# Kernel tuning notes

Hardware: AMD Instinct MI355X
Metric: run time of the kernel (lower is better)

The kernel has to match this reference:

```python
import jax, jax.numpy as jnp
import numpy as np

B, N, K = 8192, 2048, 4  # batch, nodes, neighbors (original: 45, 168, 4)


def _collect_and_transfer(x, adj):
    # x: (B, N), adj: (N, K) int indices of neighbors.
    # Original builds, per node i, a (B, K) block of gathered neighbor values,
    # stacks to (N, B, K), then raw-reshapes (view) to (B, 1, K, N).
    g = jnp.transpose(x[:, adj], (1, 0, 2))   # (N, B, K)
    return g.reshape(x.shape[0], 1, K, adj.shape[0])  # memory reinterpretation, as in .view


def reference(x, label, adj, conv_w, conv_b, lin_w, lin_b):
    a = jnp.concatenate([_collect_and_transfer(x, adj),
                         _collect_and_transfer(label, adj)], axis=1)  # (B, 2, K, N)
    # Conv2d(2 -> 1, kernel=(1,4), stride=(1,4)): (B, 1, K, N//4)
    y = jax.lax.conv_general_dilated(
        a, conv_w, window_strides=(1, 4), padding='VALID',
        dimension_numbers=('NCHW', 'OIHW', 'NCHW'))
    y = jax.nn.relu(y + conv_b[None, :, None, None])
    y = y.reshape(B, N)              # K * (N//4) == N
    return y @ lin_w.T + lin_b       # Linear(N, N)


def setup_inputs() -> dict:
    key = jax.random.key(0)
    k1, k2, k3, k4, k5 = jax.random.split(key, 5)
    return {
        'x': jax.random.normal(k1, (B, N), dtype=jnp.float32),
        'label': jax.random.normal(k2, (B, N), dtype=jnp.float32),
        'adj': jax.random.randint(k3, (N, K), 0, N, dtype=jnp.int32),
        'conv_w': jax.random.normal(k4, (1, 2, 1, 4), dtype=jnp.float32) * 0.1,
        'conv_b': jnp.zeros((1,), dtype=jnp.float32),
        'lin_w': jax.random.normal(k5, (N, N), dtype=jnp.float32) * 0.02,
        'lin_b': jnp.zeros((N,), dtype=jnp.float32),
    }
```

## Files before the change

### kernel.cpp

```cpp
#include <hip/hip_runtime.h>

typedef __bf16 bf16;
typedef bf16 bf16x8 __attribute__((ext_vector_type(8)));
typedef float f32x4 __attribute__((ext_vector_type(4)));
typedef unsigned short ushort;
typedef ushort ushort4v __attribute__((ext_vector_type(4)));

#define BB 8192
#define NN 2048

__device__ __forceinline__ void async16(const void* g, void* l) {
    __builtin_amdgcn_global_load_lds(
        (__attribute__((address_space(1))) void*)(void*)g,
        (__attribute__((address_space(3))) void*)l,
        16, 0, 0);
}

__global__ __launch_bounds__(256) void conv_gather(
    const float* __restrict__ x, const float* __restrict__ label,
    const int* __restrict__ adj, const float* __restrict__ cw,
    const float* __restrict__ cb, bf16* __restrict__ V) {
    __shared__ float4 sxl[NN];
    const int bb0 = blockIdx.x * 2;
    const int t   = threadIdx.x;

    const float4* x0 = (const float4*)(x     + (size_t)bb0 * NN);
    const float4* x1 = (const float4*)(x     + (size_t)(bb0 + 1) * NN);
    const float4* l0 = (const float4*)(label + (size_t)bb0 * NN);
    const float4* l1 = (const float4*)(label + (size_t)(bb0 + 1) * NN);
#pragma unroll
    for (int q = 0; q < 2; ++q) {
        int i = q * 256 + t;
        float4 a = x0[i], b = l0[i], c = x1[i], d = l1[i];
        sxl[i*4+0] = make_float4(a.x, b.x, c.x, d.x);
        sxl[i*4+1] = make_float4(a.y, b.y, c.y, d.y);
        sxl[i*4+2] = make_float4(a.z, b.z, c.z, d.z);
        sxl[i*4+3] = make_float4(a.w, b.w, c.w, d.w);
    }
    const float w0 = cw[0], w1 = cw[1], w2 = cw[2], w3 = cw[3];
    const float w4 = cw[4], w5 = cw[5], w6 = cw[6], w7 = cw[7];
    const float bias = cb[0];

    const int4* adj4 = (const int4*)adj;
    int4 a[8];
#pragma unroll
    for (int j = 0; j < 8; ++j) a[j] = adj4[t * 8 + j];

    __syncthreads();

    bf16 o0[8], o1[8];
#pragma unroll
    for (int j = 0; j < 8; ++j) {
        int4 aa = a[j];
        float4 p0 = sxl[aa.x];
        float4 p1 = sxl[aa.y];
        float4 p2 = sxl[aa.z];
        float4 p3 = sxl[aa.w];
        float v0 = bias
                 + w0 * p0.x + w1 * p1.x + w2 * p2.x + w3 * p3.x
                 + w4 * p0.y + w5 * p1.y + w6 * p2.y + w7 * p3.y;
        float v1 = bias
                 + w0 * p0.z + w1 * p1.z + w2 * p2.z + w3 * p3.z
                 + w4 * p0.w + w5 * p1.w + w6 * p2.w + w7 * p3.w;
        o0[j] = (bf16)fmaxf(v0, 0.0f);
        o1[j] = (bf16)fmaxf(v1, 0.0f);
    }
    *(bf16x8*)(V + (size_t)bb0 * NN + t * 8)       = *(const bf16x8*)o0;
    *(bf16x8*)(V + (size_t)(bb0 + 1) * NN + t * 8) = *(const bf16x8*)o1;
}

__global__ __launch_bounds__(256) void transp_cvtw(
    const ushort* __restrict__ V, ushort* __restrict__ Y,
    const float* __restrict__ W, bf16* __restrict__ Wb) {
    const int b = blockIdx.x;
    if (b >= 4096) {
        size_t i = (size_t)(b - 4096) * 256 + threadIdx.x;
        float4 v0 = ((const float4*)W)[i * 2 + 0];
        float4 v1 = ((const float4*)W)[i * 2 + 1];
        bf16x8 o;
        o[0] = (bf16)v0.x; o[1] = (bf16)v0.y; o[2] = (bf16)v0.z; o[3] = (bf16)v0.w;
        o[4] = (bf16)v1.x; o[5] = (bf16)v1.y; o[6] = (bf16)v1.z; o[7] = (bf16)v1.w;
        ((bf16x8*)Wb)[i] = o;
        return;
    }
    __shared__ ushort tile[64][68];
    const int g0 = (b & 31) * 64;
    const int p0 = (b >> 5) * 64;
    const int c  = threadIdx.x & 15;
    const int r4 = threadIdx.x >> 4;

#pragma unroll
    for (int pass = 0; pass < 4; ++pass) {
        int r = pass * 16 + r4;
        ushort4v v = *(const ushort4v*)(V + (size_t)(p0 + r) * NN + g0 + c * 4);
        *(ushort4v*)&tile[r][c * 4] = v;
    }
    __syncthreads();
#pragma unroll
    for (int pass = 0; pass < 4; ++pass) {
        int r = pass * 16 + r4;
        ushort4v o;
        o.x = tile[c * 4 + 0][r];
        o.y = tile[c * 4 + 1][r];
        o.z = tile[c * 4 + 2][r];
        o.w = tile[c * 4 + 3][r];
        *(ushort4v*)(Y + (size_t)(g0 + r) * BB + p0 + c * 4) = o;
    }
}

__global__ __launch_bounds__(256) void gemm_bt(
    const bf16* __restrict__ A, const bf16* __restrict__ W,
    const float* __restrict__ bias, float* __restrict__ out) {
    __shared__ __attribute__((aligned(16))) bf16 sA[2][128 * 32];
    __shared__ __attribute__((aligned(16))) bf16 sB[2][128 * 32];

    const int t    = threadIdx.x;
    const int lane = t & 63;
    const int wv   = t >> 6;
    const int wm   = wv & 1;
    const int wn   = wv >> 1;
    const int m0   = blockIdx.x * 128;
    const int n0   = blockIdx.y * 128;

    f32x4 acc[4][4] = {};

    const int r  = t >> 2;
    const int c8 = (t & 3) * 8;
    const bf16* gA0 = A + (size_t)(m0 + r)      * 2048 + c8;
    const bf16* gA1 = A + (size_t)(m0 + r + 64) * 2048 + c8;
    const bf16* gB0 = W + (size_t)(n0 + r)      * 2048 + c8;
    const bf16* gB1 = W + (size_t)(n0 + r + 64) * 2048 + c8;
    bf16* lA0[2], *lA1[2], *lB0[2], *lB1[2];
#pragma unroll
    for (int s = 0; s < 2; ++s) {
        lA0[s] = sA[s] + (wv * 16)      * 32;
        lA1[s] = sA[s] + (64 + wv * 16) * 32;
        lB0[s] = sB[s] + (wv * 16)      * 32;
        lB1[s] = sB[s] + (64 + wv * 16) * 32;
    }

    const int quad = lane >> 4;
    const int l16  = lane & 15;
    const int foff = (wm * 64 + l16) * 32 + quad * 8;
    const int goff = (wn * 64 + l16) * 32 + quad * 8;

    for (int k0 = 0; k0 < 2048; k0 += 64) {
#pragma unroll
        for (int s = 0; s < 2; ++s) {
            async16(gA0 + k0 + s * 32, lA0[s]);
            async16(gA1 + k0 + s * 32, lA1[s]);
            async16(gB0 + k0 + s * 32, lB0[s]);
            async16(gB1 + k0 + s * 32, lB1[s]);
        }
        __syncthreads();

#pragma unroll
        for (int s = 0; s < 2; ++s) {
            const bf16* fA = sA[s] + foff;
            const bf16* fB = sB[s] + goff;
            bf16x8 af[4], bfr[4];
#pragma unroll
            for (int i = 0; i < 4; ++i) af[i]  = *(const bf16x8*)(fA + i * 16 * 32);
#pragma unroll
            for (int j = 0; j < 4; ++j) bfr[j] = *(const bf16x8*)(fB + j * 16 * 32);
#pragma unroll
            for (int i = 0; i < 4; ++i)
#pragma unroll
                for (int j = 0; j < 4; ++j)
                    acc[i][j] = __builtin_amdgcn_mfma_f32_16x16x32_bf16(
                        af[i], bfr[j], acc[i][j], 0, 0, 0);
        }
        __syncthreads();
    }

#pragma unroll
    for (int j = 0; j < 4; ++j) {
        int col = n0 + wn * 64 + j * 16 + l16;
        float bcol = bias[col];
#pragma unroll
        for (int i = 0; i < 4; ++i) {
            int rowb = m0 + wm * 64 + i * 16 + quad * 4;
#pragma unroll
            for (int rr = 0; rr < 4; ++rr) {
                out[(size_t)(rowb + rr) * 2048 + col] = acc[i][j][rr] + bcol;
            }
        }
    }
}

extern "C" void kernel_launch(void* const* d_in, const int* in_sizes, int n_in,
                              void* d_out, int out_size, void* d_ws, size_t ws_size,
                              hipStream_t stream) {
    (void)in_sizes; (void)n_in; (void)out_size; (void)ws_size;
    const float* x     = (const float*)d_in[0];
    const float* label = (const float*)d_in[1];
    const int*   adj   = (const int*)d_in[2];
    const float* cw    = (const float*)d_in[3];
    const float* cb    = (const float*)d_in[4];
    const float* lw    = (const float*)d_in[5];
    const float* lb    = (const float*)d_in[6];
    float* out = (float*)d_out;

    bf16* V  = (bf16*)d_out;
    bf16* Y2 = (bf16*)d_ws;
    bf16* Wb = (bf16*)((char*)d_ws + (size_t)2048 * 8192 * 2);

    conv_gather<<<BB / 2, 256, 0, stream>>>(x, label, adj, cw, cb, V);
    transp_cvtw<<<6144, 256, 0, stream>>>((const ushort*)V, (ushort*)Y2,
                                          lw, Wb);
    gemm_bt<<<dim3(64, 16), 256, 0, stream>>>(Y2, Wb, lb, out);
}
```

Baseline: 281.7 us.

## Rewrite GEMM with 256x256 tiles, 8 waves, swizzled LDS and interleaved prefetch

The GEMM moves from 128x128 tiles with 4 waves to 256x256 tiles with 8 waves and K-steps of 64. It uses XOR-swizzled LDS layouts and a hand-scheduled double buffer that interleaves async global-to-LDS loads with MFMA phases, using explicit barriers, waitcnts and setprio. The gather kernel also XOR-swizzles its shared-memory table to reduce bank conflicts on random neighbour reads. The larger tile raises arithmetic intensity, but the grid shrinks to 256 blocks and register pressure rises, which may leave CUs underused.

```diff
diff --git a/kernel.cpp b/kernel.cpp
--- a/kernel.cpp
+++ b/kernel.cpp
@@ -32,10 +32,12 @@
     for (int q = 0; q < 2; ++q) {
         int i = q * 256 + t;
         float4 a = x0[i], b = l0[i], c = x1[i], d = l1[i];
-        sxl[i*4+0] = make_float4(a.x, b.x, c.x, d.x);
-        sxl[i*4+1] = make_float4(a.y, b.y, c.y, d.y);
-        sxl[i*4+2] = make_float4(a.z, b.z, c.z, d.z);
-        sxl[i*4+3] = make_float4(a.w, b.w, c.w, d.w);
+        int n0i = i * 4;
+        int sx  = (i >> 1) & 7;
+        sxl[(n0i + 0) ^ sx] = make_float4(a.x, b.x, c.x, d.x);
+        sxl[(n0i + 1) ^ sx] = make_float4(a.y, b.y, c.y, d.y);
+        sxl[(n0i + 2) ^ sx] = make_float4(a.z, b.z, c.z, d.z);
+        sxl[(n0i + 3) ^ sx] = make_float4(a.w, b.w, c.w, d.w);
     }
     const float w0 = cw[0], w1 = cw[1], w2 = cw[2], w3 = cw[3];
     const float w4 = cw[4], w5 = cw[5], w6 = cw[6], w7 = cw[7];
@@ -52,10 +54,10 @@
 #pragma unroll
     for (int j = 0; j < 8; ++j) {
         int4 aa = a[j];
-        float4 p0 = sxl[aa.x];
-        float4 p1 = sxl[aa.y];
-        float4 p2 = sxl[aa.z];
-        float4 p3 = sxl[aa.w];
+        float4 p0 = sxl[aa.x ^ ((aa.x >> 3) & 7)];
+        float4 p1 = sxl[aa.y ^ ((aa.y >> 3) & 7)];
+        float4 p2 = sxl[aa.z ^ ((aa.z >> 3) & 7)];
+        float4 p3 = sxl[aa.w ^ ((aa.w >> 3) & 7)];
         float v0 = bias
                  + w0 * p0.x + w1 * p1.x + w2 * p2.x + w3 * p3.x
                  + w4 * p0.y + w5 * p1.y + w6 * p2.y + w7 * p3.y;
@@ -108,84 +110,182 @@
     }
 }
 
-__global__ __launch_bounds__(256) void gemm_bt(
+__global__ __launch_bounds__(512, 2) void gemm_bt(
     const bf16* __restrict__ A, const bf16* __restrict__ W,
     const float* __restrict__ bias, float* __restrict__ out) {
-    __shared__ __attribute__((aligned(16))) bf16 sA[2][128 * 32];
-    __shared__ __attribute__((aligned(16))) bf16 sB[2][128 * 32];
+    __shared__ __attribute__((aligned(16))) bf16 sA[2][16384];
+    __shared__ __attribute__((aligned(16))) bf16 sB[2][16384];
 
     const int t    = threadIdx.x;
     const int lane = t & 63;
     const int wv   = t >> 6;
     const int wm   = wv & 1;
     const int wn   = wv >> 1;
-    const int m0   = blockIdx.x * 128;
-    const int n0   = blockIdx.y * 128;
-
-    f32x4 acc[4][4] = {};
-
-    const int r  = t >> 2;
-    const int c8 = (t & 3) * 8;
-    const bf16* gA0 = A + (size_t)(m0 + r)      * 2048 + c8;
-    const bf16* gA1 = A + (size_t)(m0 + r + 64) * 2048 + c8;
-    const bf16* gB0 = W + (size_t)(n0 + r)      * 2048 + c8;
-    const bf16* gB1 = W + (size_t)(n0 + r + 64) * 2048 + c8;
-    bf16* lA0[2], *lA1[2], *lB0[2], *lB1[2];
-#pragma unroll
-    for (int s = 0; s < 2; ++s) {
-        lA0[s] = sA[s] + (wv * 16)      * 32;
-        lA1[s] = sA[s] + (64 + wv * 16) * 32;
-        lB0[s] = sB[s] + (wv * 16)      * 32;
-        lB1[s] = sB[s] + (64 + wv * 16) * 32;
-    }
-
-    const int quad = lane >> 4;
     const int l16  = lane & 15;
-    const int foff = (wm * 64 + l16) * 32 + quad * 8;
-    const int goff = (wn * 64 + l16) * 32 + quad * 8;
-
-    for (int k0 = 0; k0 < 2048; k0 += 64) {
-#pragma unroll
-        for (int s = 0; s < 2; ++s) {
-            async16(gA0 + k0 + s * 32, lA0[s]);
-            async16(gA1 + k0 + s * 32, lA1[s]);
-            async16(gB0 + k0 + s * 32, lB0[s]);
-            async16(gB1 + k0 + s * 32, lB1[s]);
+    const int l4   = lane >> 4;
+
+    const int bx = blockIdx.x >> 3;
+    const int by = blockIdx.x & 7;
+    const int m0 = bx * 256;
+    const int n0 = by * 256;
+
+    const int r8  = t >> 3;
+    const int c8  = ((t & 7) ^ (r8 & 7)) * 8;
+    const int dst = t * 8;
+
+    const int sw    = l16 & 7;
+    const int aOff0 = (wm * 128 + l16) * 64 + ((l4    ) ^ sw) * 8;
+    const int aOff1 = (wm * 128 + l16) * 64 + ((l4 + 4) ^ sw) * 8;
+    const int bOff0 = (wn * 64  + l16) * 64 + ((l4    ) ^ sw) * 8;
+    const int bOff1 = (wn * 64  + l16) * 64 + ((l4 + 4) ^ sw) * 8;
+
+    f32x4  acc[8][4] = {};
+    bf16x8 aR[4][2], bR[4][2];
+
+#define GBAR()  asm volatile("s_barrier" ::: "memory")
+#define LGKM0() asm volatile("s_waitcnt lgkmcnt(0)" ::: "memory")
+#define VMW4()  asm volatile("s_waitcnt vmcnt(4)" ::: "memory")
+#define VMW0()  asm volatile("s_waitcnt vmcnt(0)" ::: "memory")
+
+#define STG(G, rb, kt, lp) do {                                           \
+        const bf16* _s = (G) + (size_t)((rb) + r8) * 2048 + (kt) + c8;    \
+        async16(_s, (lp) + dst);                                          \
+        async16(_s + (size_t)64 * 2048, (lp) + 4096 + dst);               \
+    } while (0)
+
+#define LDA(sp, mh) do {                                                  \
+        const bf16* _p = (sp) + (mh) * 4096;                              \
+        aR[0][0] = *(const bf16x8*)(_p + aOff0);                          \
+        aR[0][1] = *(const bf16x8*)(_p + aOff1);                          \
+        aR[1][0] = *(const bf16x8*)(_p + 1024 + aOff0);                   \
+        aR[1][1] = *(const bf16x8*)(_p + 1024 + aOff1);                   \
+        aR[2][0] = *(const bf16x8*)(_p + 2048 + aOff0);                   \
+        aR[2][1] = *(const bf16x8*)(_p + 2048 + aOff1);                   \
+        aR[3][0] = *(const bf16x8*)(_p + 3072 + aOff0);                   \
+        aR[3][1] = *(const bf16x8*)(_p + 3072 + aOff1);                   \
+    } while (0)
+
+#define LDB(sp, nh) do {                                                  \
+        const bf16* _p = (sp) + (nh) * 2048;                              \
+        bR[(nh)*2+0][0] = *(const bf16x8*)(_p + bOff0);                   \
+        bR[(nh)*2+0][1] = *(const bf16x8*)(_p + bOff1);                   \
+        bR[(nh)*2+1][0] = *(const bf16x8*)(_p + 1024 + bOff0);            \
+        bR[(nh)*2+1][1] = *(const bf16x8*)(_p + 1024 + bOff1);            \
+    } while (0)
+
+#define MM(mh, nh) do {                                                   \
+        __builtin_amdgcn_s_setprio(1);                                    \
+        _Pragma("unroll")                                                 \
+        for (int _mf = 0; _mf < 4; ++_mf)                                 \
+            _Pragma("unroll")                                             \
+            for (int _nf = 0; _nf < 2; ++_nf) {                           \
+                acc[(mh)*4+_mf][(nh)*2+_nf] =                             \
+                    __builtin_amdgcn_mfma_f32_16x16x32_bf16(              \
+                        aR[_mf][0], bR[(nh)*2+_nf][0],                    \
+                        acc[(mh)*4+_mf][(nh)*2+_nf], 0, 0, 0);            \
+                acc[(mh)*4+_mf][(nh)*2+_nf] =                             \
+                    __builtin_amdgcn_mfma_f32_16x16x32_bf16(              \
+                        aR[_mf][1], bR[(nh)*2+_nf][1],                    \
+                        acc[(mh)*4+_mf][(nh)*2+_nf], 0, 0, 0);            \
+            }                                                             \
+        __builtin_amdgcn_s_setprio(0);                                    \
+    } while (0)
+
+    bf16* const sA0 = &sA[0][0]; bf16* const sA1 = &sA[1][0];
+    bf16* const sB0 = &sB[0][0]; bf16* const sB1 = &sB[1][0];
+
+    STG(A, m0,       0,  sA0);
+    STG(A, m0 + 128, 0,  sA0 + 8192);
+    STG(W, n0,       0,  sB0);
+    STG(W, n0 + 128, 0,  sB0 + 8192);
+    STG(W, n0,       64, sB1);
+    STG(W, n0 + 128, 64, sB1 + 8192);
+    VMW4();
+    GBAR();
+
+    for (int i = 0; i < 15; ++i) {
+        const int kb = i * 128;
+        LDA(sA0, 0); LDB(sB0, 0);
+        STG(A, m0, kb + 64, sA1);
+        GBAR(); LGKM0();
+        MM(0, 0);
+        GBAR();
+        LDB(sB0, 1);
+        STG(A, m0 + 128, kb + 64, sA1 + 8192);
+        GBAR(); LGKM0();
+        MM(0, 1);
+        GBAR();
+        LDA(sA0, 1);
+        STG(W, n0, kb + 128, sB0);
+        GBAR(); LGKM0();
+        MM(1, 0);
+        GBAR();
+        STG(W, n0 + 128, kb + 128, sB0 + 8192);
+        GBAR(); LGKM0();
+        MM(1, 1);
+        VMW4();
+        GBAR();
+        LDA(sA1, 0); LDB(sB1, 0);
+        STG(A, m0, kb + 128, sA0);
+        GBAR(); LGKM0();
+        MM(0, 0);
+        GBAR();
+        LDB(sB1, 1);
+        STG(A, m0 + 128, kb + 128, sA0 + 8192);
+        GBAR(); LGKM0();
+        MM(0, 1);
+        GBAR();
+        LDA(sA1, 1);
+        STG(W, n0, kb + 192, sB1);
+        GBAR(); LGKM0();
+        MM(1, 0);
+        GBAR();
+        STG(W, n0 + 128, kb + 192, sB1 + 8192);
+        GBAR(); LGKM0();
+        MM(1, 1);
+        VMW4();
+        GBAR();
+    }
+
+    LDA(sA0, 0); LDB(sB0, 0);
+    STG(A, m0, 1984, sA1);
+    GBAR(); LGKM0(); MM(0, 0); GBAR();
+    LDB(sB0, 1);
+    STG(A, m0 + 128, 1984, sA1 + 8192);
+    GBAR(); LGKM0(); MM(0, 1); GBAR();
+    LDA(sA0, 1);
+    GBAR(); LGKM0(); MM(1, 0); GBAR();
+    GBAR(); LGKM0(); MM(1, 1);
+    VMW0();
+    GBAR();
+    LDA(sA1, 0); LDB(sB1, 0);
+    GBAR(); LGKM0(); MM(0, 0); GBAR();
+    LDB(sB1, 1);
+    GBAR(); LGKM0(); MM(0, 1); GBAR();
+    LDA(sA1, 1);
+    GBAR(); LGKM0(); MM(1, 0); GBAR();
+    GBAR(); LGKM0(); MM(1, 1);
+
+#pragma unroll
+    for (int nf = 0; nf < 4; ++nf) {
+        const int col = n0 + wn * 64 + nf * 16 + l16;
+        const float bc = bias[col];
+#pragma unroll
+        for (int mf = 0; mf < 8; ++mf) {
+            const size_t row = (size_t)(m0 + wm * 128 + mf * 16 + l4 * 4);
+#pragma unroll
+            for (int rr = 0; rr < 4; ++rr)
+                out[(row + rr) * 2048 + col] = acc[mf][nf][rr] + bc;
         }
-        __syncthreads();
-
-#pragma unroll
-        for (int s = 0; s < 2; ++s) {
-            const bf16* fA = sA[s] + foff;
-            const bf16* fB = sB[s] + goff;
-            bf16x8 af[4], bfr[4];
-#pragma unroll
-            for (int i = 0; i < 4; ++i) af[i]  = *(const bf16x8*)(fA + i * 16 * 32);
-#pragma unroll
-            for (int j = 0; j < 4; ++j) bfr[j] = *(const bf16x8*)(fB + j * 16 * 32);
-#pragma unroll
-            for (int i = 0; i < 4; ++i)
-#pragma unroll
-                for (int j = 0; j < 4; ++j)
-                    acc[i][j] = __builtin_amdgcn_mfma_f32_16x16x32_bf16(
-                        af[i], bfr[j], acc[i][j], 0, 0, 0);
-        }
-        __syncthreads();
-    }
-
-#pragma unroll
-    for (int j = 0; j < 4; ++j) {
-        int col = n0 + wn * 64 + j * 16 + l16;
-        float bcol = bias[col];
-#pragma unroll
-        for (int i = 0; i < 4; ++i) {
-            int rowb = m0 + wm * 64 + i * 16 + quad * 4;
-#pragma unroll
-            for (int rr = 0; rr < 4; ++rr) {
-                out[(size_t)(rowb + rr) * 2048 + col] = acc[i][j][rr] + bcol;
-            }
-        }
-    }
+    }
+#undef STG
+#undef LDA
+#undef LDB
+#undef MM
+#undef GBAR
+#undef LGKM0
+#undef VMW4
+#undef VMW0
 }
 
 extern "C" void kernel_launch(void* const* d_in, const int* in_sizes, int n_in,
@@ -208,5 +308,5 @@
     conv_gather<<<BB / 2, 256, 0, stream>>>(x, label, adj, cw, cb, V);
     transp_cvtw<<<6144, 256, 0, stream>>>((const ushort*)V, (ushort*)Y2,
                                           lw, Wb);
-    gemm_bt<<<dim3(64, 16), 256, 0, stream>>>(Y2, Wb, lb, out);
-}
+    gemm_bt<<<dim3(256), 512, 0, stream>>>(Y2, Wb, lb, out);
+}
```

After: 278.7 us. About the same (-1.1%).
